# Kernel optimization log

Measured on AMD Instinct MI355X. Metric: run time of the kernel, lower is better.

The kernel has to match this reference:

```python
import jax, jax.numpy as jnp
import numpy as np

EPS = 1e-5
H = 12  # num_heads

def ste_sign(x):
    # forward: sign(x) in {-1,+1}; backward: grad passes where |x|<1 (clip STE)
    c = jnp.clip(x, -1.0, 1.0)
    s = jnp.where(x >= 0, 1.0, -1.0).astype(x.dtype)
    return c + jax.lax.stop_gradient(s - c)

def bin_w(w):
    # adaptive per-output-channel scaling: alpha = mean|w| (detached), weight = alpha*sign(w)
    alpha = jax.lax.stop_gradient(jnp.mean(jnp.abs(w), axis=1, keepdims=True))
    return alpha * ste_sign(w)

def layernorm(x, g, b):
    mu = jnp.mean(x, axis=-1, keepdims=True)
    var = jnp.var(x, axis=-1, keepdims=True)
    return (x - mu) * jax.lax.rsqrt(var + EPS) * g + b

def setup_inputs():
    key = jax.random.key(0)
    ks = jax.random.split(key, 6)
    B, N, C, hid = 8, 1024, 768, 3072
    s = 0.02
    return {
        "x": jax.random.normal(ks[0], (B, N, C), jnp.float32),
        "ln1_g": jnp.ones((C,), jnp.float32),
        "ln1_b": jnp.zeros((C,), jnp.float32),
        "w_qkv": jax.random.normal(ks[1], (3 * C, C), jnp.float32) * s,
        "w_proj": jax.random.normal(ks[2], (C, C), jnp.float32) * s,
        "b_proj": jnp.zeros((C,), jnp.float32),
        "ls1_g": 1e-5 * jnp.ones((C,), jnp.float32),
        "ln2_g": jnp.ones((C,), jnp.float32),
        "ln2_b": jnp.zeros((C,), jnp.float32),
        "w_fc1": jax.random.normal(ks[3], (hid, C), jnp.float32) * s,
        "b_fc1": jnp.zeros((hid,), jnp.float32),
        "w_fc2": jax.random.normal(ks[4], (C, hid), jnp.float32) * s,
        "b_fc2": jnp.zeros((C,), jnp.float32),
        "ls2_g": 1e-5 * jnp.ones((C,), jnp.float32),
    }

def reference(x, ln1_g, ln1_b, w_qkv, w_proj, b_proj, ls1_g, ln2_g, ln2_b, w_fc1, b_fc1, w_fc2, b_fc2, ls2_g):
    B, N, C = x.shape
    hd = C // H
    scale = hd ** -0.5
    # --- binarized attention ---
    h = layernorm(x, ln1_g, ln1_b)
    qkv = jnp.einsum('bnc,oc->bno', ste_sign(h), bin_w(w_qkv))        # 1w1a qkv proj
    qkv = qkv.reshape(B, N, 3, H, hd).transpose(2, 0, 3, 1, 4)        # [3,B,H,N,hd]
    bqkv = ste_sign(qkv)                                              # BinaryQuantizer
    q, k, v = bqkv[0], bqkv[1], bqkv[2]
    attn = jnp.einsum('bhnd,bhmd->bhnm', q, k) * scale                # [B,H,N,N]
    sm = jax.nn.softmax(attn, axis=-1)
    abin = (attn > 0).astype(x.dtype)                                 # SoftmaxBinaryQuantizer fwd value
    attn_eff = sm + jax.lax.stop_gradient(abin - sm)                  # STE: fwd=binary, bwd=softmax
    o = jnp.einsum('bhnm,bhmd->bhnd', attn_eff, v)
    o = o.transpose(0, 2, 1, 3).reshape(B, N, C)
    o = jnp.einsum('bnc,oc->bno', ste_sign(o), bin_w(w_proj)) + b_proj
    x = x + ls1_g * o
    # --- binary MLP (1-bit weight, 32-bit activation) ---
    h2 = layernorm(x, ln2_g, ln2_b)
    m = jax.nn.gelu(jnp.einsum('bnc,hc->bnh', h2, bin_w(w_fc1)) + b_fc1, approximate=False)
    m = jnp.einsum('bnh,ch->bnc', m, bin_w(w_fc2)) + b_fc2
    return x + ls2_g * m
```

## Files before the change

kernel.cpp:

```cpp
#include <hip/hip_runtime.h>

#define NTOK 8192
#define CDIM 768
#define HIDD 3072
#define NQKV 2304
#define SEQL 1024
#define NHEAD 12

typedef int i32x4 __attribute__((ext_vector_type(4)));
typedef float f32x4 __attribute__((ext_vector_type(4)));
typedef signed char sc16 __attribute__((ext_vector_type(16)));

__device__ __forceinline__ void gload_lds16(const void* g, void* l) {
    __builtin_amdgcn_global_load_lds(
        (const __attribute__((address_space(1))) unsigned int*)g,
        (__attribute__((address_space(3))) unsigned int*)l, 16, 0, 0);
}

__global__ void sign_w_kernel(const float* __restrict__ w, signed char* __restrict__ ws, int n) {
    int i = blockIdx.x * blockDim.x + threadIdx.x;
    int stride = gridDim.x * blockDim.x;
    for (; i < n; i += stride)
        ws[i] = (w[i] >= 0.0f) ? 1 : -1;
}

template<bool PERM>
__global__ void __launch_bounds__(256) signalpha_kernel(const float* __restrict__ w,
                                                        signed char* __restrict__ ws,
                                                        float* __restrict__ alpha, int K) {
    int row = blockIdx.x;
    const float* wr = w + (size_t)row * K;
    signed char* wsr = ws + (size_t)row * K;
    float s = 0.f;
    for (int i = threadIdx.x; i < K; i += 256) {
        float v = wr[i];
        int ip = PERM ? ((i & ~63) | (((i & 15) << 2) | ((i >> 4) & 3))) : i;
        wsr[ip] = (v >= 0.f) ? 1 : -1;
        s += fabsf(v);
    }
    for (int off = 32; off > 0; off >>= 1) s += __shfl_down(s, off);
    __shared__ float red[4];
    if ((threadIdx.x & 63) == 0) red[threadIdx.x >> 6] = s;
    __syncthreads();
    if (threadIdx.x == 0) alpha[row] = (red[0] + red[1] + red[2] + red[3]) / (float)K;
}

__global__ void __launch_bounds__(256) ln_sign_kernel(const float* __restrict__ x, const float* __restrict__ g,
                                                      const float* __restrict__ b, signed char* __restrict__ out) {
    int row = blockIdx.x;
    const float* xr = x + (size_t)row * CDIM;
    float v0 = xr[threadIdx.x], v1 = xr[threadIdx.x + 256], v2 = xr[threadIdx.x + 512];
    float s = v0 + v1 + v2, s2 = v0 * v0 + v1 * v1 + v2 * v2;
    for (int off = 32; off > 0; off >>= 1) { s += __shfl_down(s, off); s2 += __shfl_down(s2, off); }
    __shared__ float red[8];
    if ((threadIdx.x & 63) == 0) { red[threadIdx.x >> 6] = s; red[4 + (threadIdx.x >> 6)] = s2; }
    __syncthreads();
    float ts = red[0] + red[1] + red[2] + red[3];
    float t2 = red[4] + red[5] + red[6] + red[7];
    float mu = ts * (1.0f / CDIM);
    float var = t2 * (1.0f / CDIM) - mu * mu;
    float rstd = rsqrtf(var + 1e-5f);
    signed char* orow = out + (size_t)row * CDIM;
    float vv[3] = {v0, v1, v2};
#pragma unroll
    for (int p = 0; p < 3; p++) {
        int i = threadIdx.x + p * 256;
        float val = (vv[p] - mu) * rstd * g[i] + b[i];
        orow[i] = (val >= 0.f) ? 1 : -1;
    }
}

__global__ void __launch_bounds__(256) proj_ln_fuse(
    const float* __restrict__ acc, const float* __restrict__ x,
    const float* __restrict__ ap, const float* __restrict__ bp, const float* __restrict__ ls1,
    const float* __restrict__ g2, const float* __restrict__ b2,
    float* __restrict__ x1out, signed char* __restrict__ h2, float* __restrict__ rowscale) {
    int row = blockIdx.x;
    const float* ar = acc + (size_t)row * CDIM;
    const float* xr = x + (size_t)row * CDIM;
    float* x1r = x1out + (size_t)row * CDIM;
    float v[3];
    float s = 0.f, s2 = 0.f;
#pragma unroll
    for (int p = 0; p < 3; p++) {
        int i = threadIdx.x + p * 256;
        float t = xr[i] + ls1[i] * (ap[i] * ar[i] + bp[i]);
        x1r[i] = t;
        v[p] = t;
        s += t; s2 += t * t;
    }
    for (int off = 32; off > 0; off >>= 1) { s += __shfl_down(s, off); s2 += __shfl_down(s2, off); }
    __shared__ float red[8];
    __shared__ float redm[4];
    if ((threadIdx.x & 63) == 0) { red[threadIdx.x >> 6] = s; red[4 + (threadIdx.x >> 6)] = s2; }
    __syncthreads();
    float ts = red[0] + red[1] + red[2] + red[3];
    float t2 = red[4] + red[5] + red[6] + red[7];
    float mu = ts * (1.0f / CDIM);
    float var = t2 * (1.0f / CDIM) - mu * mu;
    float rstd = rsqrtf(var + 1e-5f);
    float a[3];
    float mx = 0.f;
#pragma unroll
    for (int p = 0; p < 3; p++) {
        int i = threadIdx.x + p * 256;
        a[p] = (v[p] - mu) * rstd * g2[i] + b2[i];
        mx = fmaxf(mx, fabsf(a[p]));
    }
    for (int off = 32; off > 0; off >>= 1) mx = fmaxf(mx, __shfl_down(mx, off));
    if ((threadIdx.x & 63) == 0) redm[threadIdx.x >> 6] = mx;
    __syncthreads();
    float rmax = fmaxf(fmaxf(redm[0], redm[1]), fmaxf(redm[2], redm[3]));
    rmax = fmaxf(rmax, 1e-20f);
    float inv = 127.f / rmax;
    signed char* orow = h2 + (size_t)row * CDIM;
#pragma unroll
    for (int p = 0; p < 3; p++)
        orow[threadIdx.x + p * 256] = (signed char)__float2int_rn(a[p] * inv);
    if (threadIdx.x == 0) rowscale[row] = rmax * (1.f / 127.f);
}

__global__ void __launch_bounds__(256) fc2_fuse(
    const float* __restrict__ acc, const float* __restrict__ af2,
    const float* __restrict__ bf2, const float* __restrict__ ls2, float* __restrict__ out) {
    int n4 = NTOK * CDIM / 4;
    int stride = gridDim.x * 256;
    for (int i4 = blockIdx.x * 256 + threadIdx.x; i4 < n4; i4 += stride) {
        int c4 = (i4 << 2) % CDIM;
        f32x4 a = *(const f32x4*)&af2[c4];
        f32x4 b = *(const f32x4*)&bf2[c4];
        f32x4 l = *(const f32x4*)&ls2[c4];
        f32x4 vacc = *(const f32x4*)&acc[(size_t)i4 * 4];
        f32x4 o = *(const f32x4*)&out[(size_t)i4 * 4];
        o = o + l * (a * vacc + b);
        *(f32x4*)&out[(size_t)i4 * 4] = o;
    }
}

enum { EPI_GELU = 2, EPI_QKV = 3 };
#define MSCALE_INV 16.0f

template<int EPI>
__global__ void __launch_bounds__(512, 4) gemm_i8(
    const signed char* __restrict__ A, const signed char* __restrict__ B,
    int M, int N, int K,
    const float* __restrict__ alpha, const float* __restrict__ bias,
    const float* __restrict__ rowscale,
    signed char* __restrict__ outB, signed char* __restrict__ vtB)
{
    __shared__ __align__(16) char lds_raw[3 * (256 + 128) * 64];
    auto As = (signed char (*)[256][64])lds_raw;
    auto Bs = (signed char (*)[128][64])(lds_raw + 3 * 256 * 64);

    const int tid = threadIdx.x, ln = tid & 63, w = tid >> 6;
    const int wm = w >> 1, wn = w & 1;
    const int lq = ln & 15, khi = ln >> 4;

    const int nwg = gridDim.x * gridDim.y;
    const int id = blockIdx.y * gridDim.x + blockIdx.x;
    const int nid = (id & 7) * (nwg >> 3) + (id >> 3);
    const int bxs = nid % gridDim.x, bys = nid / gridDim.x;
    const int bm = bys * 256, bn = bxs * 128;

    const i32x4 iz = {0, 0, 0, 0};
    i32x4 acc[4][4];
#pragma unroll
    for (int m = 0; m < 4; m++)
#pragma unroll
        for (int n = 0; n < 4; n++) acc[m][n] = iz;

    const int srow = tid >> 2, scol = (tid & 3) * 16;
    const int ssrc = ((tid & 3) ^ ((srow >> 1) & 3)) * 16;
    const int sa = 16 * (khi ^ ((lq >> 1) & 3));

    auto STAGE = [&](int p, int k0) {
        gload_lds16(A + (size_t)(bm + srow) * K + k0 + ssrc, &As[p][srow][scol]);
        gload_lds16(A + (size_t)(bm + 128 + srow) * K + k0 + ssrc, &As[p][128 + srow][scol]);
        gload_lds16(B + (size_t)(bn + srow) * K + k0 + ssrc, &Bs[p][srow][scol]);
    };
    auto COMPUTE = [&](int p, bool prefetch, int knext) {
        i32x4 aF[4], bF[4];
#pragma unroll
        for (int m = 0; m < 4; m++) aF[m] = *(const i32x4*)&As[p][wm * 64 + m * 16 + lq][sa];
#pragma unroll
        for (int n = 0; n < 4; n++) bF[n] = *(const i32x4*)&Bs[p][wn * 64 + n * 16 + lq][sa];
        if (prefetch) STAGE((p + 2) % 3, knext);
        __builtin_amdgcn_s_setprio(1);
#pragma unroll
        for (int m = 0; m < 4; m++)
#pragma unroll
            for (int n = 0; n < 4; n++)
                acc[m][n] = __builtin_amdgcn_mfma_i32_16x16x64_i8(aF[m], bF[n], acc[m][n], 0, 0, 0);
        __builtin_amdgcn_s_setprio(0);
    };

    const int nst = K >> 6;
    STAGE(0, 0);
    STAGE(1, 64);
#pragma unroll 1
    for (int t = 0; t < nst - 1; t++) {
        asm volatile("s_waitcnt vmcnt(3)" ::: "memory");
        asm volatile("s_waitcnt lgkmcnt(0)" ::: "memory");
        __builtin_amdgcn_s_barrier();
        COMPUTE(t % 3, t + 2 < nst, (t + 2) << 6);
    }
    asm volatile("s_waitcnt vmcnt(0)" ::: "memory");
    asm volatile("s_waitcnt lgkmcnt(0)" ::: "memory");
    __builtin_amdgcn_s_barrier();
    COMPUTE((nst - 1) % 3, false, 0);

    const int r0 = bm + wm * 64;
    const int c0 = bn + wn * 64;

    if constexpr (EPI == EPI_GELU) {
        float al[4], bi[4];
#pragma unroll
        for (int n = 0; n < 4; n++) {
            al[n] = alpha[c0 + n * 16 + lq];
            bi[n] = bias[c0 + n * 16 + lq];
        }
#pragma unroll
        for (int m = 0; m < 4; m++)
#pragma unroll
            for (int i = 0; i < 4; i++) {
                int r = r0 + m * 16 + khi * 4 + i;
                float rs = rowscale[r];
                unsigned pk = 0;
#pragma unroll
                for (int n = 0; n < 4; n++) {
                    float t = al[n] * ((float)acc[m][n][i] * rs) + bi[n];
                    float y2 = 1.5957691f * t + 0.07135481f * t * t * t;
                    float ge = t * __builtin_amdgcn_rcpf(1.0f + __expf(-y2));
                    float qf = fminf(fmaxf(ge * MSCALE_INV, -127.f), 127.f);
                    pk |= (unsigned)(unsigned char)(signed char)__float2int_rn(qf) << (8 * n);
                }
                *(unsigned*)(outB + (size_t)r * N + c0 + lq * 4) = pk;
            }
    } else {
        if (c0 < 1536) {
#pragma unroll
            for (int m = 0; m < 4; m++)
#pragma unroll
                for (int i = 0; i < 4; i++) {
                    int r = r0 + m * 16 + khi * 4 + i;
                    unsigned pk = 0;
#pragma unroll
                    for (int n = 0; n < 4; n++)
                        pk |= (unsigned)(unsigned char)(signed char)((acc[m][n][i] >= 0) ? 1 : -1) << (8 * n);
                    *(unsigned*)(outB + (size_t)r * 1536 + c0 + lq * 4) = pk;
                }
        } else {
#pragma unroll
            for (int m = 0; m < 4; m++)
#pragma unroll
                for (int n = 0; n < 4; n++) {
                    int cg = c0 + n * 16 + lq - 1536;
                    int hh = cg >> 6, dd = cg & 63;
                    int rb = r0 + m * 16 + khi * 4;
                    unsigned pk = 0;
#pragma unroll
                    for (int i = 0; i < 4; i++)
                        pk |= (unsigned)(unsigned char)(signed char)((acc[m][n][i] >= 0) ? 1 : -1) << (8 * i);
                    *(unsigned*)(vtB + (((size_t)(rb >> 10) * NHEAD + hh) * 64 + dd) * SEQL + (rb & 1023)) = pk;
                }
        }
    }
}

__global__ void __launch_bounds__(256) gemm_acc(
    const signed char* __restrict__ A, const signed char* __restrict__ B,
    int N, int K, float ascale, float* __restrict__ outF)
{
    __shared__ __align__(16) char lds_raw[4 * (128 + 64) * 64];
    auto As = (signed char (*)[128][64])lds_raw;
    auto Bs = (signed char (*)[64][64])(lds_raw + 4 * 128 * 64);

    const int tid = threadIdx.x, ln = tid & 63, w = tid >> 6;
    const int wm = w >> 1, wn = w & 1;
    const int lq = ln & 15, khi = ln >> 4;

    const int nwg = gridDim.x * gridDim.y;
    const int id = blockIdx.y * gridDim.x + blockIdx.x;
    const int nid = (id & 7) * (nwg >> 3) + (id >> 3);
    const int bxs = nid % gridDim.x, bys = nid / gridDim.x;
    const int bm = bys * 128, bn = bxs * 64;

    const i32x4 iz = {0, 0, 0, 0};
    i32x4 acc[4][2];
#pragma unroll
    for (int m = 0; m < 4; m++)
#pragma unroll
        for (int n = 0; n < 2; n++) acc[m][n] = iz;

    const int srow = tid >> 2, scol = (tid & 3) * 16;
    const int ssrc = ((tid & 3) ^ ((srow >> 1) & 3)) * 16;
    const int sa = 16 * (khi ^ ((lq >> 1) & 3));

    auto STAGE = [&](int p, int k0) {
        gload_lds16(A + (size_t)(bm + srow) * K + k0 + ssrc, &As[p][srow][scol]);
        gload_lds16(A + (size_t)(bm + 64 + srow) * K + k0 + ssrc, &As[p][64 + srow][scol]);
        gload_lds16(B + (size_t)(bn + srow) * K + k0 + ssrc, &Bs[p][srow][scol]);
    };
    auto COMPUTE = [&](int p, bool prefetch, int knext) {
        i32x4 aF[4], bF[2];
#pragma unroll
        for (int m = 0; m < 4; m++) aF[m] = *(const i32x4*)&As[p][wm * 64 + m * 16 + lq][sa];
#pragma unroll
        for (int n = 0; n < 2; n++) bF[n] = *(const i32x4*)&Bs[p][wn * 32 + n * 16 + lq][sa];
        if (prefetch) STAGE((p + 3) & 3, knext);
        __builtin_amdgcn_s_setprio(1);
#pragma unroll
        for (int m = 0; m < 4; m++)
#pragma unroll
            for (int n = 0; n < 2; n++)
                acc[m][n] = __builtin_amdgcn_mfma_i32_16x16x64_i8(aF[m], bF[n], acc[m][n], 0, 0, 0);
        __builtin_amdgcn_s_setprio(0);
    };

    const int nst = K >> 6;
    STAGE(0, 0);
    STAGE(1, 64);
    STAGE(2, 128);
#pragma unroll 1
    for (int t = 0; t < nst; t++) {
        int rem = nst - 1 - t;
        if (rem >= 2)      asm volatile("s_waitcnt vmcnt(6)" ::: "memory");
        else if (rem == 1) asm volatile("s_waitcnt vmcnt(3)" ::: "memory");
        else               asm volatile("s_waitcnt vmcnt(0)" ::: "memory");
        asm volatile("s_waitcnt lgkmcnt(0)" ::: "memory");
        __builtin_amdgcn_s_barrier();
        COMPUTE(t & 3, t + 3 < nst, (t + 3) << 6);
    }

    __syncthreads();
    float (*Cf)[68] = (float (*)[68])lds_raw;
#pragma unroll
    for (int m = 0; m < 4; m++)
#pragma unroll
        for (int n = 0; n < 2; n++)
#pragma unroll
            for (int i = 0; i < 4; i++)
                Cf[wm * 64 + m * 16 + khi * 4 + i][wn * 32 + n * 16 + lq] =
                    (float)acc[m][n][i] * ascale;
    __syncthreads();
#pragma unroll
    for (int p = 0; p < 8; p++) {
        int idx = p * 256 + tid;
        int row = idx >> 4, c4 = (idx & 15) * 4;
        f32x4 v4 = *(const f32x4*)&Cf[row][c4];
        *(f32x4*)&outF[(size_t)(bm + row) * N + bn + c4] = v4;
    }
}

__global__ void __launch_bounds__(256) attn_v2(const signed char* __restrict__ qk,
                                               const signed char* __restrict__ vt,
                                               signed char* __restrict__ a2) {
    const int id = blockIdx.x;
    const int nid = (id & 7) * 96 + (id >> 3);
    const int bh = nid >> 3, qb = nid & 7;
    const int b = bh / NHEAD, h = bh % NHEAD;
    const int tid = threadIdx.x, ln = tid & 63, w = tid >> 6;
    const int lq = ln & 15, khi = ln >> 4;

    __shared__ signed char Ks[64][80];
    __shared__ signed char Vts[64][80];
    __shared__ signed char Pw[4][32][80];

    const size_t tokbase = (size_t)b * SEQL;
    const int q0 = qb * 128 + w * 32;
    const int str = tid >> 2, stc = (tid & 3) * 16;
    const size_t vtrow = ((size_t)bh * 64 + str) * SEQL;

    i32x4 qfrag[2];
#pragma unroll
    for (int qf = 0; qf < 2; qf++)
        qfrag[qf] = *(const i32x4*)(qk + (tokbase + q0 + qf * 16 + lq) * 1536 + h * 64 + khi * 16);

    const i32x4 iz = {0, 0, 0, 0};
    i32x4 o[2][4];
#pragma unroll
    for (int qf = 0; qf < 2; qf++)
#pragma unroll
        for (int df = 0; df < 4; df++) o[qf][df] = iz;

    auto LOADJ = [&](int j, sc16& kr, sc16& vr) {
        kr = *(const sc16*)(qk + (tokbase + j * 64 + str) * 1536 + 768 + h * 64 + stc);
        vr = *(const sc16*)(vt + vtrow + j * 64 + stc);
    };
    auto STORE = [&](const sc16& kr, const sc16& vr) {
        *(sc16*)&Ks[str][stc] = kr;
        *(sc16*)&Vts[str][stc] = vr;
    };
    auto COMPUTE = [&]() {
        i32x4 kfrag[4];
#pragma unroll
        for (int kf = 0; kf < 4; kf++)
            kfrag[kf] = *(const i32x4*)&Ks[kf * 16 + lq][khi * 16];
#pragma unroll
        for (int kf = 0; kf < 4; kf++) {
#pragma unroll
            for (int qf = 0; qf < 2; qf++) {
                i32x4 st = __builtin_amdgcn_mfma_i32_16x16x64_i8(kfrag[kf], qfrag[qf], iz, 0, 0, 0);
                unsigned pb = (st[0] > 0 ? 1u : 0u) | (st[1] > 0 ? 0x100u : 0u) |
                              (st[2] > 0 ? 0x10000u : 0u) | (st[3] > 0 ? 0x1000000u : 0u);
                *(unsigned*)&Pw[w][qf * 16 + lq][kf * 16 + khi * 4] = pb;
            }
        }
        i32x4 pa[2];
#pragma unroll
        for (int qf = 0; qf < 2; qf++)
            pa[qf] = *(const i32x4*)&Pw[w][qf * 16 + lq][khi * 16];
#pragma unroll
        for (int df = 0; df < 4; df++) {
            i32x4 vfr = *(const i32x4*)&Vts[df * 16 + lq][khi * 16];
#pragma unroll
            for (int qf = 0; qf < 2; qf++)
                o[qf][df] = __builtin_amdgcn_mfma_i32_16x16x64_i8(pa[qf], vfr, o[qf][df], 0, 0, 0);
        }
    };

    sc16 ka, va, kb, vb;
    LOADJ(0, ka, va);
#pragma unroll 1
    for (int jj = 0; jj < 16; jj += 2) {
        __syncthreads();
        STORE(ka, va);
        __syncthreads();
        LOADJ(jj + 1, kb, vb);
        COMPUTE();
        __syncthreads();
        STORE(kb, vb);
        __syncthreads();
        if (jj + 2 < 16) LOADJ(jj + 2, ka, va);
        COMPUTE();
    }

#pragma unroll
    for (int qf = 0; qf < 2; qf++)
#pragma unroll
        for (int i = 0; i < 4; i++) {
            int qrow = q0 + qf * 16 + khi * 4 + i;
            unsigned pk = 0;
#pragma unroll
            for (int df = 0; df < 4; df++)
                pk |= (unsigned)(unsigned char)(signed char)((o[qf][df][i] >= 0) ? 1 : -1) << (8 * df);
            *(unsigned*)(a2 + (tokbase + qrow) * CDIM + h * 64 + lq * 4) = pk;
        }
}

static const size_t OFF_WQKV  = 0;
static const size_t OFF_WPROJ = 1769472;
static const size_t OFF_WFC1  = 2359296;
static const size_t OFF_WFC2  = 4718592;
static const size_t OFF_APROJ = 7077888;
static const size_t OFF_AFC1  = 7080960;
static const size_t OFF_AFC2  = 7093248;
static const size_t OFF_H2SC  = 7096320;
static const size_t OFF_QK    = 7129088;
static const size_t OFF_VT    = 19712000;
static const size_t OFF_A1    = 26003456;
static const size_t OFF_A2    = 32294912;
static const size_t OFF_M1    = 38586368;
static const size_t OFF_H2    = 63752192;
static const size_t OFF_CACC  = OFF_QK;

extern "C" void kernel_launch(void* const* d_in, const int* in_sizes, int n_in,
                              void* d_out, int out_size, void* d_ws, size_t ws_size,
                              hipStream_t stream) {
    const float* x      = (const float*)d_in[0];
    const float* ln1_g  = (const float*)d_in[1];
    const float* ln1_b  = (const float*)d_in[2];
    const float* w_qkv  = (const float*)d_in[3];
    const float* w_proj = (const float*)d_in[4];
    const float* b_proj = (const float*)d_in[5];
    const float* ls1_g  = (const float*)d_in[6];
    const float* ln2_g  = (const float*)d_in[7];
    const float* ln2_b  = (const float*)d_in[8];
    const float* w_fc1  = (const float*)d_in[9];
    const float* b_fc1  = (const float*)d_in[10];
    const float* w_fc2  = (const float*)d_in[11];
    const float* b_fc2  = (const float*)d_in[12];
    const float* ls2_g  = (const float*)d_in[13];
    float* out = (float*)d_out;

    char* ws = (char*)d_ws;
    signed char* wqkv_s  = (signed char*)(ws + OFF_WQKV);
    signed char* wproj_s = (signed char*)(ws + OFF_WPROJ);
    signed char* wfc1_s  = (signed char*)(ws + OFF_WFC1);
    signed char* wfc2_s  = (signed char*)(ws + OFF_WFC2);
    float* a_proj  = (float*)(ws + OFF_APROJ);
    float* a_fc1   = (float*)(ws + OFF_AFC1);
    float* a_fc2   = (float*)(ws + OFF_AFC2);
    float* h2scale = (float*)(ws + OFF_H2SC);
    signed char* qk   = (signed char*)(ws + OFF_QK);
    signed char* vt   = (signed char*)(ws + OFF_VT);
    signed char* a1   = (signed char*)(ws + OFF_A1);
    signed char* a2   = (signed char*)(ws + OFF_A2);
    signed char* m1   = (signed char*)(ws + OFF_M1);
    signed char* h2   = (signed char*)(ws + OFF_H2);
    float* cacc = (float*)(ws + OFF_CACC);

    sign_w_kernel<<<512, 256, 0, stream>>>(w_qkv, wqkv_s, NQKV * CDIM);
    signalpha_kernel<true><<<CDIM, 256, 0, stream>>>(w_proj, wproj_s, a_proj, CDIM);
    signalpha_kernel<false><<<HIDD, 256, 0, stream>>>(w_fc1,  wfc1_s,  a_fc1,  CDIM);
    signalpha_kernel<true><<<CDIM, 256, 0, stream>>>(w_fc2,  wfc2_s,  a_fc2,  HIDD);

    ln_sign_kernel<<<NTOK, 256, 0, stream>>>(x, ln1_g, ln1_b, a1);

    gemm_i8<EPI_QKV><<<dim3(NQKV / 128, NTOK / 256), 512, 0, stream>>>(
        a1, wqkv_s, NTOK, NQKV, CDIM, nullptr, nullptr, nullptr, qk, vt);

    attn_v2<<<768, 256, 0, stream>>>(qk, vt, a2);

    gemm_acc<<<dim3(CDIM / 64, NTOK / 128), 256, 0, stream>>>(
        a2, wproj_s, CDIM, CDIM, 1.0f, cacc);

    proj_ln_fuse<<<NTOK, 256, 0, stream>>>(cacc, x, a_proj, b_proj, ls1_g,
                                           ln2_g, ln2_b, out, h2, h2scale);

    gemm_i8<EPI_GELU><<<dim3(HIDD / 128, NTOK / 256), 512, 0, stream>>>(
        h2, wfc1_s, NTOK, HIDD, CDIM, a_fc1, b_fc1, h2scale, m1, nullptr);

    gemm_acc<<<dim3(CDIM / 64, NTOK / 128), 256, 0, stream>>>(
        m1, wfc2_s, CDIM, HIDD, 1.0f / MSCALE_INV, cacc);

    fc2_fuse<<<2048, 256, 0, stream>>>(cacc, a_fc2, b_fc2, ls2_g, out);
}
```

Measured before the change: 186.6 us.

## Remap workgroups so each XCD owns one batch's token range across all kernels

Changes block-to-tile mapping in the layernorm, fused epilogue, GEMM and attention kernels so that blocks landing on the same XCD (blockIdx & 7) handle a contiguous slice of tokens (one batch). This keeps each batch's activations local to one XCD's L2 across consecutive kernels and within the GEMMs. The fc2 epilogue becomes a fixed-work-per-block layout instead of a grid-stride loop, which assumes a specific grid size. The mapping assumes round-robin XCD dispatch and that the grid dimensions divide evenly by 8.

Result: no change. 185.3 us (-0.7%).

```diff
diff --git a/kernel.cpp b/kernel.cpp
--- a/kernel.cpp
+++ b/kernel.cpp
@@ -47,7 +47,7 @@
 
 __global__ void __launch_bounds__(256) ln_sign_kernel(const float* __restrict__ x, const float* __restrict__ g,
                                                       const float* __restrict__ b, signed char* __restrict__ out) {
-    int row = blockIdx.x;
+    int row = ((blockIdx.x & 7) << 10) | (blockIdx.x >> 3);
     const float* xr = x + (size_t)row * CDIM;
     float v0 = xr[threadIdx.x], v1 = xr[threadIdx.x + 256], v2 = xr[threadIdx.x + 512];
     float s = v0 + v1 + v2, s2 = v0 * v0 + v1 * v1 + v2 * v2;
@@ -75,7 +75,7 @@
     const float* __restrict__ ap, const float* __restrict__ bp, const float* __restrict__ ls1,
     const float* __restrict__ g2, const float* __restrict__ b2,
     float* __restrict__ x1out, signed char* __restrict__ h2, float* __restrict__ rowscale) {
-    int row = blockIdx.x;
+    int row = ((blockIdx.x & 7) << 10) | (blockIdx.x >> 3);
     const float* ar = acc + (size_t)row * CDIM;
     const float* xr = x + (size_t)row * CDIM;
     float* x1r = x1out + (size_t)row * CDIM;
@@ -123,17 +123,19 @@
 __global__ void __launch_bounds__(256) fc2_fuse(
     const float* __restrict__ acc, const float* __restrict__ af2,
     const float* __restrict__ bf2, const float* __restrict__ ls2, float* __restrict__ out) {
-    int n4 = NTOK * CDIM / 4;
-    int stride = gridDim.x * 256;
-    for (int i4 = blockIdx.x * 256 + threadIdx.x; i4 < n4; i4 += stride) {
-        int c4 = (i4 << 2) % CDIM;
+    const int xcd = blockIdx.x & 7, j = blockIdx.x >> 3;
+    const size_t base = (size_t)xcd * 196608 + (size_t)j * 768;
+#pragma unroll
+    for (int p = 0; p < 3; p++) {
+        size_t i4 = base + p * 256 + threadIdx.x;
+        int c4 = (int)((i4 << 2) % CDIM);
         f32x4 a = *(const f32x4*)&af2[c4];
         f32x4 b = *(const f32x4*)&bf2[c4];
         f32x4 l = *(const f32x4*)&ls2[c4];
-        f32x4 vacc = *(const f32x4*)&acc[(size_t)i4 * 4];
-        f32x4 o = *(const f32x4*)&out[(size_t)i4 * 4];
+        f32x4 vacc = *(const f32x4*)&acc[i4 * 4];
+        f32x4 o = *(const f32x4*)&out[i4 * 4];
         o = o + l * (a * vacc + b);
-        *(f32x4*)&out[(size_t)i4 * 4] = o;
+        *(f32x4*)&out[i4 * 4] = o;
     }
 }
 
@@ -156,10 +158,11 @@
     const int wm = w >> 1, wn = w & 1;
     const int lq = ln & 15, khi = ln >> 4;
 
-    const int nwg = gridDim.x * gridDim.y;
     const int id = blockIdx.y * gridDim.x + blockIdx.x;
-    const int nid = (id & 7) * (nwg >> 3) + (id >> 3);
-    const int bxs = nid % gridDim.x, bys = nid / gridDim.x;
+    const int xcd = id & 7, j = id >> 3;
+    const int mpx = gridDim.y >> 3;
+    const int bys = xcd * mpx + j / gridDim.x;
+    const int bxs = j % gridDim.x;
     const int bm = bys * 256, bn = bxs * 128;
 
     const i32x4 iz = {0, 0, 0, 0};
@@ -279,10 +282,11 @@
     const int wm = w >> 1, wn = w & 1;
     const int lq = ln & 15, khi = ln >> 4;
 
-    const int nwg = gridDim.x * gridDim.y;
     const int id = blockIdx.y * gridDim.x + blockIdx.x;
-    const int nid = (id & 7) * (nwg >> 3) + (id >> 3);
-    const int bxs = nid % gridDim.x, bys = nid / gridDim.x;
+    const int xcd = id & 7, j = id >> 3;
+    const int mpx = gridDim.y >> 3;
+    const int bys = xcd * mpx + j / gridDim.x;
+    const int bxs = j % gridDim.x;
     const int bm = bys * 128, bn = bxs * 64;
 
     const i32x4 iz = {0, 0, 0, 0};
@@ -356,9 +360,10 @@
                                                const signed char* __restrict__ vt,
                                                signed char* __restrict__ a2) {
     const int id = blockIdx.x;
-    const int nid = (id & 7) * 96 + (id >> 3);
-    const int bh = nid >> 3, qb = nid & 7;
-    const int b = bh / NHEAD, h = bh % NHEAD;
+    const int b = id & 7;
+    const int j = id >> 3;
+    const int h = j >> 3, qb = j & 7;
+    const int bh = b * NHEAD + h;
     const int tid = threadIdx.x, ln = tid & 63, w = tid >> 6;
     const int lq = ln & 15, khi = ln >> 4;
 
@@ -383,9 +388,9 @@
 #pragma unroll
         for (int df = 0; df < 4; df++) o[qf][df] = iz;
 
-    auto LOADJ = [&](int j, sc16& kr, sc16& vr) {
-        kr = *(const sc16*)(qk + (tokbase + j * 64 + str) * 1536 + 768 + h * 64 + stc);
-        vr = *(const sc16*)(vt + vtrow + j * 64 + stc);
+    auto LOADJ = [&](int jj, sc16& kr, sc16& vr) {
+        kr = *(const sc16*)(qk + (tokbase + jj * 64 + str) * 1536 + 768 + h * 64 + stc);
+        vr = *(const sc16*)(vt + vtrow + jj * 64 + stc);
     };
     auto STORE = [&](const sc16& kr, const sc16& vr) {
         *(sc16*)&Ks[str][stc] = kr;
```

## Fuse residual epilogues into int8 GEMMs and carry mid-residual in bf16

Applied to the files above, without the earlier changes.

The proj and fc2 GEMMs now apply alpha, bias, layer-scale and the residual add in their epilogue and write the result directly, removing the fp32 accumulator round trips and the separate fc2_fuse pass. The intermediate residual x1 is stored as bf16 and a slimmer LN2 kernel reads it to produce the quantized h2. The GEMM pipeline depth drops from four to three LDS stages, and residual tiles are prefetched into registers before the main loop. bf16 storage of x1 loses precision in the final output, and the extra registers for the residual prefetch may reduce occupancy.

Result: faster. 169.5 us (-9.2%).

```diff
diff --git a/kernel.cpp b/kernel.cpp
--- a/kernel.cpp
+++ b/kernel.cpp
@@ -10,6 +10,16 @@
 typedef int i32x4 __attribute__((ext_vector_type(4)));
 typedef float f32x4 __attribute__((ext_vector_type(4)));
 typedef signed char sc16 __attribute__((ext_vector_type(16)));
+typedef unsigned short us4 __attribute__((ext_vector_type(4)));
+
+__device__ __forceinline__ unsigned short f32_to_bf16(float f) {
+    unsigned int u = __float_as_uint(f);
+    u += 0x7FFFu + ((u >> 16) & 1u);
+    return (unsigned short)(u >> 16);
+}
+__device__ __forceinline__ float bf16_to_f32(unsigned short h) {
+    return __uint_as_float(((unsigned)h) << 16);
+}
 
 __device__ __forceinline__ void gload_lds16(const void* g, void* l) {
     __builtin_amdgcn_global_load_lds(
@@ -70,25 +80,15 @@
     }
 }
 
-__global__ void __launch_bounds__(256) proj_ln_fuse(
-    const float* __restrict__ acc, const float* __restrict__ x,
-    const float* __restrict__ ap, const float* __restrict__ bp, const float* __restrict__ ls1,
-    const float* __restrict__ g2, const float* __restrict__ b2,
-    float* __restrict__ x1out, signed char* __restrict__ h2, float* __restrict__ rowscale) {
+__global__ void __launch_bounds__(256) ln2q_kernel(const unsigned short* __restrict__ x, const float* __restrict__ g,
+                                                   const float* __restrict__ b, signed char* __restrict__ out,
+                                                   float* __restrict__ rowscale) {
     int row = blockIdx.x;
-    const float* ar = acc + (size_t)row * CDIM;
-    const float* xr = x + (size_t)row * CDIM;
-    float* x1r = x1out + (size_t)row * CDIM;
-    float v[3];
-    float s = 0.f, s2 = 0.f;
-#pragma unroll
-    for (int p = 0; p < 3; p++) {
-        int i = threadIdx.x + p * 256;
-        float t = xr[i] + ls1[i] * (ap[i] * ar[i] + bp[i]);
-        x1r[i] = t;
-        v[p] = t;
-        s += t; s2 += t * t;
-    }
+    const unsigned short* xr = x + (size_t)row * CDIM;
+    float v0 = bf16_to_f32(xr[threadIdx.x]);
+    float v1 = bf16_to_f32(xr[threadIdx.x + 256]);
+    float v2 = bf16_to_f32(xr[threadIdx.x + 512]);
+    float s = v0 + v1 + v2, s2 = v0 * v0 + v1 * v1 + v2 * v2;
     for (int off = 32; off > 0; off >>= 1) { s += __shfl_down(s, off); s2 += __shfl_down(s2, off); }
     __shared__ float red[8];
     __shared__ float redm[4];
@@ -99,42 +99,21 @@
     float mu = ts * (1.0f / CDIM);
     float var = t2 * (1.0f / CDIM) - mu * mu;
     float rstd = rsqrtf(var + 1e-5f);
-    float a[3];
-    float mx = 0.f;
-#pragma unroll
-    for (int p = 0; p < 3; p++) {
-        int i = threadIdx.x + p * 256;
-        a[p] = (v[p] - mu) * rstd * g2[i] + b2[i];
-        mx = fmaxf(mx, fabsf(a[p]));
-    }
+    float a0 = (v0 - mu) * rstd * g[threadIdx.x] + b[threadIdx.x];
+    float a1 = (v1 - mu) * rstd * g[threadIdx.x + 256] + b[threadIdx.x + 256];
+    float a2v = (v2 - mu) * rstd * g[threadIdx.x + 512] + b[threadIdx.x + 512];
+    float mx = fmaxf(fabsf(a0), fmaxf(fabsf(a1), fabsf(a2v)));
     for (int off = 32; off > 0; off >>= 1) mx = fmaxf(mx, __shfl_down(mx, off));
     if ((threadIdx.x & 63) == 0) redm[threadIdx.x >> 6] = mx;
     __syncthreads();
     float rmax = fmaxf(fmaxf(redm[0], redm[1]), fmaxf(redm[2], redm[3]));
     rmax = fmaxf(rmax, 1e-20f);
     float inv = 127.f / rmax;
-    signed char* orow = h2 + (size_t)row * CDIM;
-#pragma unroll
-    for (int p = 0; p < 3; p++)
-        orow[threadIdx.x + p * 256] = (signed char)__float2int_rn(a[p] * inv);
+    signed char* orow = out + (size_t)row * CDIM;
+    orow[threadIdx.x]       = (signed char)__float2int_rn(a0 * inv);
+    orow[threadIdx.x + 256] = (signed char)__float2int_rn(a1 * inv);
+    orow[threadIdx.x + 512] = (signed char)__float2int_rn(a2v * inv);
     if (threadIdx.x == 0) rowscale[row] = rmax * (1.f / 127.f);
-}
-
-__global__ void __launch_bounds__(256) fc2_fuse(
-    const float* __restrict__ acc, const float* __restrict__ af2,
-    const float* __restrict__ bf2, const float* __restrict__ ls2, float* __restrict__ out) {
-    int n4 = NTOK * CDIM / 4;
-    int stride = gridDim.x * 256;
-    for (int i4 = blockIdx.x * 256 + threadIdx.x; i4 < n4; i4 += stride) {
-        int c4 = (i4 << 2) % CDIM;
-        f32x4 a = *(const f32x4*)&af2[c4];
-        f32x4 b = *(const f32x4*)&bf2[c4];
-        f32x4 l = *(const f32x4*)&ls2[c4];
-        f32x4 vacc = *(const f32x4*)&acc[(size_t)i4 * 4];
-        f32x4 o = *(const f32x4*)&out[(size_t)i4 * 4];
-        o = o + l * (a * vacc + b);
-        *(f32x4*)&out[(size_t)i4 * 4] = o;
-    }
 }
 
 enum { EPI_GELU = 2, EPI_QKV = 3 };
@@ -267,13 +246,19 @@
     }
 }
 
-__global__ void __launch_bounds__(256) gemm_acc(
+template<bool FINAL>
+__global__ void __launch_bounds__(256) gemm_resid(
     const signed char* __restrict__ A, const signed char* __restrict__ B,
-    int N, int K, float ascale, float* __restrict__ outF)
+    int N, int K,
+    const float* __restrict__ alpha, const float* __restrict__ bias,
+    const float* __restrict__ ls,
+    const float* __restrict__ residF, const unsigned short* __restrict__ residH,
+    float ascale,
+    float* __restrict__ outF, unsigned short* __restrict__ outH)
 {
-    __shared__ __align__(16) char lds_raw[4 * (128 + 64) * 64];
+    __shared__ __align__(16) char lds_raw[3 * (128 + 64) * 64];
     auto As = (signed char (*)[128][64])lds_raw;
-    auto Bs = (signed char (*)[64][64])(lds_raw + 4 * 128 * 64);
+    auto Bs = (signed char (*)[64][64])(lds_raw + 3 * 128 * 64);
 
     const int tid = threadIdx.x, ln = tid & 63, w = tid >> 6;
     const int wm = w >> 1, wn = w & 1;
@@ -285,6 +270,20 @@
     const int bxs = nid % gridDim.x, bys = nid / gridDim.x;
     const int bm = bys * 128, bn = bxs * 64;
 
+    const int erow = tid >> 4;
+    const int ec4 = (tid & 15) * 4;
+    f32x4 a4 = *(const f32x4*)&alpha[bn + ec4];
+    f32x4 b4 = *(const f32x4*)&bias[bn + ec4];
+    f32x4 l4 = *(const f32x4*)&ls[bn + ec4];
+    f32x4 rF[8];
+    us4 rH[8];
+#pragma unroll
+    for (int p = 0; p < 8; p++) {
+        size_t g = (size_t)(bm + p * 16 + erow) * N + bn + ec4;
+        if constexpr (FINAL) rH[p] = *(const us4*)&residH[g];
+        else                 rF[p] = *(const f32x4*)&residF[g];
+    }
+
     const i32x4 iz = {0, 0, 0, 0};
     i32x4 acc[4][2];
 #pragma unroll
@@ -307,7 +306,7 @@
         for (int m = 0; m < 4; m++) aF[m] = *(const i32x4*)&As[p][wm * 64 + m * 16 + lq][sa];
 #pragma unroll
         for (int n = 0; n < 2; n++) bF[n] = *(const i32x4*)&Bs[p][wn * 32 + n * 16 + lq][sa];
-        if (prefetch) STAGE((p + 3) & 3, knext);
+        if (prefetch) STAGE((p + 2) % 3, knext);
         __builtin_amdgcn_s_setprio(1);
 #pragma unroll
         for (int m = 0; m < 4; m++)
@@ -320,17 +319,17 @@
     const int nst = K >> 6;
     STAGE(0, 0);
     STAGE(1, 64);
-    STAGE(2, 128);
 #pragma unroll 1
-    for (int t = 0; t < nst; t++) {
-        int rem = nst - 1 - t;
-        if (rem >= 2)      asm volatile("s_waitcnt vmcnt(6)" ::: "memory");
-        else if (rem == 1) asm volatile("s_waitcnt vmcnt(3)" ::: "memory");
-        else               asm volatile("s_waitcnt vmcnt(0)" ::: "memory");
+    for (int t = 0; t < nst - 1; t++) {
+        asm volatile("s_waitcnt vmcnt(3)" ::: "memory");
         asm volatile("s_waitcnt lgkmcnt(0)" ::: "memory");
         __builtin_amdgcn_s_barrier();
-        COMPUTE(t & 3, t + 3 < nst, (t + 3) << 6);
-    }
+        COMPUTE(t % 3, t + 2 < nst, (t + 2) << 6);
+    }
+    asm volatile("s_waitcnt vmcnt(0)" ::: "memory");
+    asm volatile("s_waitcnt lgkmcnt(0)" ::: "memory");
+    __builtin_amdgcn_s_barrier();
+    COMPUTE((nst - 1) % 3, false, 0);
 
     __syncthreads();
     float (*Cf)[68] = (float (*)[68])lds_raw;
@@ -345,10 +344,22 @@
     __syncthreads();
 #pragma unroll
     for (int p = 0; p < 8; p++) {
-        int idx = p * 256 + tid;
-        int row = idx >> 4, c4 = (idx & 15) * 4;
-        f32x4 v4 = *(const f32x4*)&Cf[row][c4];
-        *(f32x4*)&outF[(size_t)(bm + row) * N + bn + c4] = v4;
+        int row = p * 16 + erow;
+        f32x4 v4 = *(const f32x4*)&Cf[row][ec4];
+        size_t g = (size_t)(bm + row) * N + bn + ec4;
+        if constexpr (FINAL) {
+            f32x4 r;
+            r.x = bf16_to_f32(rH[p].x); r.y = bf16_to_f32(rH[p].y);
+            r.z = bf16_to_f32(rH[p].z); r.w = bf16_to_f32(rH[p].w);
+            f32x4 o4 = r + l4 * (a4 * v4 + b4);
+            *(f32x4*)&outF[g] = o4;
+        } else {
+            f32x4 o4 = rF[p] + l4 * (a4 * v4 + b4);
+            us4 h;
+            h.x = f32_to_bf16(o4.x); h.y = f32_to_bf16(o4.y);
+            h.z = f32_to_bf16(o4.z); h.w = f32_to_bf16(o4.w);
+            *(us4*)&outH[g] = h;
+        }
     }
 }
 
@@ -462,7 +473,7 @@
 static const size_t OFF_A2    = 32294912;
 static const size_t OFF_M1    = 38586368;
 static const size_t OFF_H2    = 63752192;
-static const size_t OFF_CACC  = OFF_QK;
+static const size_t OFF_X1B   = OFF_QK;
 
 extern "C" void kernel_launch(void* const* d_in, const int* in_sizes, int n_in,
                               void* d_out, int out_size, void* d_ws, size_t ws_size,
@@ -498,7 +509,7 @@
     signed char* a2   = (signed char*)(ws + OFF_A2);
     signed char* m1   = (signed char*)(ws + OFF_M1);
     signed char* h2   = (signed char*)(ws + OFF_H2);
-    float* cacc = (float*)(ws + OFF_CACC);
+    unsigned short* x1b = (unsigned short*)(ws + OFF_X1B);
 
     sign_w_kernel<<<512, 256, 0, stream>>>(w_qkv, wqkv_s, NQKV * CDIM);
     signalpha_kernel<true><<<CDIM, 256, 0, stream>>>(w_proj, wproj_s, a_proj, CDIM);
@@ -512,17 +523,14 @@
 
     attn_v2<<<768, 256, 0, stream>>>(qk, vt, a2);
 
-    gemm_acc<<<dim3(CDIM / 64, NTOK / 128), 256, 0, stream>>>(
-        a2, wproj_s, CDIM, CDIM, 1.0f, cacc);
-
-    proj_ln_fuse<<<NTOK, 256, 0, stream>>>(cacc, x, a_proj, b_proj, ls1_g,
-                                           ln2_g, ln2_b, out, h2, h2scale);
+    gemm_resid<false><<<dim3(CDIM / 64, NTOK / 128), 256, 0, stream>>>(
+        a2, wproj_s, CDIM, CDIM, a_proj, b_proj, ls1_g, x, nullptr, 1.0f, nullptr, x1b);
+
+    ln2q_kernel<<<NTOK, 256, 0, stream>>>(x1b, ln2_g, ln2_b, h2, h2scale);
 
     gemm_i8<EPI_GELU><<<dim3(HIDD / 128, NTOK / 256), 512, 0, stream>>>(
         h2, wfc1_s, NTOK, HIDD, CDIM, a_fc1, b_fc1, h2scale, m1, nullptr);
 
-    gemm_acc<<<dim3(CDIM / 64, NTOK / 128), 256, 0, stream>>>(
-        m1, wfc2_s, CDIM, HIDD, 1.0f / MSCALE_INV, cacc);
-
-    fc2_fuse<<<2048, 256, 0, stream>>>(cacc, a_fc2, b_fc2, ls2_g, out);
-}
+    gemm_resid<true><<<dim3(CDIM / 64, NTOK / 128), 256, 0, stream>>>(
+        m1, wfc2_s, CDIM, HIDD, a_fc2, b_fc2, ls2_g, nullptr, x1b, 1.0f / MSCALE_INV, out, nullptr);
+}
```
